# Kernel tuning notes

Hardware: AMD Instinct MI355X
Metric: run time of the kernel (lower is better)

Reference implementation:

```python
import jax, jax.numpy as jnp
import numpy as np

B, G, N = 32, 512, 512          # batch, group (POMO rollouts), problem size
EMB, H, DK = 128, 8, 16          # embedding_dim, head_num, qkv_dim (H*DK == EMB)
E, FH, K = 8, 512, 2             # num_experts, ff_hidden_dim, top-k
SQRT_EMB = 11.313708498984761    # sqrt(128), model_params['sqrt_embedding_dim']
CLIP = 10.0                      # logit_clipping


def setup_inputs() -> dict:
    key = jax.random.key(0)
    ks = jax.random.split(key, 22)
    s = 0.05
    d = {}
    d["pref"] = jax.random.uniform(ks[0], (2,), dtype=jnp.float32)
    d["graph"] = jax.random.normal(ks[1], (B, 1, EMB), dtype=jnp.float32)
    d["capacity"] = jax.random.uniform(ks[2], (B, G), dtype=jnp.float32)
    d["encoded_nodes"] = jax.random.normal(ks[3], (B, N, EMB), dtype=jnp.float32)
    d["ninf_mask"] = jnp.zeros((B, G, N), dtype=jnp.float32)
    # hyper-network MLP (note: original has NO activations between hyper_fc layers)
    d["fc1_w"] = jax.random.normal(ks[4], (256, 2)) * s
    d["fc1_b"] = jax.random.normal(ks[5], (256,)) * s
    d["fc2_w"] = jax.random.normal(ks[6], (256, 256)) * s
    d["fc2_b"] = jax.random.normal(ks[7], (256,)) * s
    d["fc3_w"] = jax.random.normal(ks[8], (8, 256)) * s
    d["fc3_b"] = jax.random.normal(ks[9], (8,)) * s
    # hyper heads producing the attention weight matrices (Linear(embd_dim=2, out), no bias)
    d["hWq"] = jax.random.normal(ks[10], ((1 + EMB) * H * DK, 2)) * 0.02
    d["hWk"] = jax.random.normal(ks[11], (EMB * H * DK, 2)) * 0.02
    d["hWv"] = jax.random.normal(ks[12], (EMB * H * DK, 2)) * 0.02
    d["hWc"] = jax.random.normal(ks[13], (EMB * H * DK, 2)) * 0.02
    # MoE combine layer: gating (token input + 8-dim pref embedding) and E expert MLPs
    d["gate_w"] = jax.random.normal(ks[14], (H * DK, E)) * s
    d["gate_pref_w"] = jax.random.normal(ks[15], (8, E)) * s
    d["e_w1"] = jax.random.normal(ks[16], (E, FH, H * DK)) * (1.0 / np.sqrt(H * DK))
    d["e_b1"] = jnp.zeros((E, FH), dtype=jnp.float32)
    d["e_w2"] = jax.random.normal(ks[17], (E, EMB, FH)) * (1.0 / np.sqrt(FH))
    d["e_b2"] = jnp.zeros((E, EMB), dtype=jnp.float32)
    d = {k2: v.astype(jnp.float32) for k2, v in d.items()}
    return d


def _heads(x):  # [B, n, H*DK] -> [B, H, n, DK]
    b, n, _ = x.shape
    return x.reshape(b, n, H, DK).transpose(0, 2, 1, 3)


def reference(pref, graph, capacity, encoded_nodes, ninf_mask,
              fc1_w, fc1_b, fc2_w, fc2_b, fc3_w, fc3_b,
              hWq, hWk, hWv, hWc,
              gate_w, gate_pref_w, e_w1, e_b1, e_w2, e_b2):
    # ---- assign(pref): hypernet generates attention weight matrices ----
    h = fc1_w @ pref + fc1_b
    h = fc2_w @ h + fc2_b
    mid = fc3_w @ h + fc3_b                      # [8] == mid_embd_pref
    Wq = (hWq @ mid[0:2]).reshape(H * DK, 1 + EMB)
    Wk = (hWk @ mid[2:4]).reshape(H * DK, EMB)
    Wv = (hWv @ mid[4:6]).reshape(H * DK, EMB)
    Wc = (hWc @ mid[6:8]).reshape(H * DK, EMB)
    # ---- set_kv ----
    k = _heads(encoded_nodes @ Wk.T)             # [B,H,N,DK]
    v = _heads(encoded_nodes @ Wv.T)
    # ---- forward ----
    inp = jnp.concatenate(
        [jnp.broadcast_to(graph, (B, G, EMB)), capacity[:, :, None]], axis=2)
    q = _heads(inp @ Wq.T)                       # [B,H,G,DK]
    score = jnp.einsum('bhgd,bhnd->bhgn', q, k) / jnp.sqrt(jnp.float32(DK))
    score = score + ninf_mask[:, None, :, :]
    attn = jax.nn.softmax(score, axis=3)
    out = jnp.einsum('bhgn,bhnd->bhgd', attn, v)
    out = out.transpose(0, 2, 1, 3).reshape(B, G, H * DK)   # [B,G,128]
    # ---- MoE combine (noisy top-k gating, deterministic at inference) ----
    logits = out @ gate_w + mid @ gate_pref_w    # [B,G,E]
    vals, idx = jax.lax.top_k(logits, K)
    gv = jax.nn.softmax(vals, axis=-1)           # softmax over selected k (T=1)
    gates = jnp.sum(jax.nn.one_hot(idx, E, dtype=out.dtype) * gv[..., None], axis=-2)
    hdn = jax.nn.relu(jnp.einsum('bgi,ehi->bgeh', out, e_w1) + e_b1)
    y = jnp.einsum('bgeh,eoh->bgeo', hdn, e_w2) + e_b2
    moe_out = jnp.einsum('bgeo,bge->bgo', y, gates)          # [B,G,EMB]
    # ---- combine + tanh-clipped masked softmax over nodes ----
    mh = moe_out @ Wc.T                           # [B,G,EMB]
    sc = jnp.einsum('bge,bne->bgn', mh, encoded_nodes) / SQRT_EMB
    probs = jax.nn.softmax(CLIP * jnp.tanh(sc) + ninf_mask, axis=2)
    return probs
```

## Files before the change

### kernel.cpp

```cpp
#include <hip/hip_runtime.h>


typedef __attribute__((ext_vector_type(8))) __bf16 bf16x8;
typedef __attribute__((ext_vector_type(4))) float f32x4;

static constexpr long OFF_MID   = 0;
static constexpr long OFF_PREFL = 8;
static constexpr long OFF_WL    = 16;
static constexpr long OFF_WKB   = 256;
static constexpr long OFF_WVB   = 8448;
static constexpr long OFF_WCB   = 16640;
static constexpr long OFF_QB    = 24832;
static constexpr long OFF_CNT   = 28928;
static constexpr long OFF_TOK   = 28936;
static constexpr long OFF_WGT   = 160008;
static constexpr long OFF_AO    = 291080;
static constexpr long OFF_MH    = 2388232;
static constexpr long OFF_ENCB  = 3436808;

__device__ __forceinline__ unsigned f2bf(float x) {
  union { float f; unsigned u; } v; v.f = x;
  return ((v.u + 0x7FFFu + ((v.u >> 16) & 1u)) >> 16) & 0xFFFFu;
}

__global__ __launch_bounds__(256)
void k_prep(const float* __restrict__ pref, const float* __restrict__ fc1w,
            const float* __restrict__ fc1b, const float* __restrict__ fc2w,
            const float* __restrict__ fc2b, const float* __restrict__ fc3w,
            const float* __restrict__ fc3b, const float* __restrict__ gpw,
            const float* __restrict__ graph,
            const float* __restrict__ hWq, const float* __restrict__ hWk,
            const float* __restrict__ hWv, const float* __restrict__ hWc,
            const float* __restrict__ ew1, const float* __restrict__ ew2,
            const float* __restrict__ enc,
            unsigned short* __restrict__ w1b, unsigned short* __restrict__ w2b,
            unsigned short* __restrict__ encb, float* __restrict__ ws) {
  const int bid = blockIdx.x;
  const int tid = threadIdx.x;
  if (bid < 3072) {
    const int i = bid*256 + tid;
    const float* src;
    unsigned short* dst;
    if (i < 131072)      { src = ew1 + (long)i*4;          dst = w1b + (long)i*4; }
    else if (i < 262144) { src = ew2 + (long)(i-131072)*4; dst = w2b + (long)(i-131072)*4; }
    else                 { src = enc + (long)(i-262144)*4; dst = encb + (long)(i-262144)*4; }
    const float4 v = *(const float4*)src;
    uint2 p;
    p.x = f2bf(v.x) | (f2bf(v.y) << 16);
    p.y = f2bf(v.z) | (f2bf(v.w) << 16);
    *(uint2*)dst = p;
    return;
  }
  __shared__ float h1[256];
  __shared__ float h2[256];
  __shared__ float mid[8];
  __shared__ float g[2][128];
  const float p0 = pref[0], p1 = pref[1];
  h1[tid] = fc1w[2*tid]*p0 + fc1w[2*tid+1]*p1 + fc1b[tid];
  __syncthreads();
  float s = 0.f;
  for (int j = 0; j < 256; ++j) s = fmaf(fc2w[tid*256+j], h1[j], s);
  h2[tid] = s + fc2b[tid];
  __syncthreads();
  if (tid < 8) {
    float s2 = 0.f;
    for (int j = 0; j < 256; ++j) s2 = fmaf(fc3w[tid*256+j], h2[j], s2);
    mid[tid] = s2 + fc3b[tid];
  }
  __syncthreads();
  if (bid < 3264) {
    const int i = (bid - 3072)*256 + tid;
    if (i < 16384) {
      ((unsigned short*)(ws + OFF_WKB))[i] =
          (unsigned short)f2bf(hWk[2*i]*mid[2] + hWk[2*i+1]*mid[3]);
    } else if (i < 32768) {
      const int j = i - 16384;
      ((unsigned short*)(ws + OFF_WVB))[j] =
          (unsigned short)f2bf(hWv[2*j]*mid[4] + hWv[2*j+1]*mid[5]);
    } else {
      const int j = i - 32768;
      ((unsigned short*)(ws + OFF_WCB))[j] =
          (unsigned short)f2bf(hWc[2*j]*mid[6] + hWc[2*j+1]*mid[7]);
    }
    return;
  }
  const int qb = bid - 3264;
  const int b0 = qb*2;
  {
    const int bb = tid >> 7, ii = tid & 127;
    g[bb][ii] = graph[(b0+bb)*128 + ii];
  }
  __syncthreads();
  const float m0 = mid[0], m1 = mid[1];
  {
    const int bb = tid >> 7, o = tid & 127;
    const float* hq = hWq + (long)o*129*2;
    float acc = 0.f;
    for (int i2 = 0; i2 < 128; ++i2) {
      const float w = hq[2*i2]*m0 + hq[2*i2+1]*m1;
      acc = fmaf(g[bb][i2], w, acc);
    }
    ws[OFF_QB + (b0+bb)*128 + o] = acc;
  }
  if (qb == 0) {
    if (tid < 8) {
      ws[OFF_MID + tid] = mid[tid];
      float s3 = 0.f;
      for (int i2 = 0; i2 < 8; ++i2) s3 = fmaf(mid[i2], gpw[i2*8 + tid], s3);
      ws[OFF_PREFL + tid] = s3;
      ((int*)(ws + OFF_CNT))[tid] = 0;
    }
    if (tid >= 16 && tid < 144) {
      const int o = tid - 16;
      ws[OFF_WL + o] = hWq[((long)o*129 + 128)*2]*m0 + hWq[((long)o*129 + 128)*2 + 1]*m1;
    }
  }
}

__device__ __forceinline__ bf16x8 ld_frag(const unsigned short* base, int row, int bytecol) {
  const int addr = row*256 + (bytecol ^ ((row & 7) << 4));
  return *(const bf16x8*)((const char*)base + addr);
}

__global__ __launch_bounds__(256)
void k_kv(const unsigned short* __restrict__ encb,
          const unsigned short* __restrict__ wkb,
          const unsigned short* __restrict__ wvb,
          unsigned short* __restrict__ Kb, unsigned short* __restrict__ Vb) {
  __shared__ unsigned short Ws[128*128];
  __shared__ unsigned short Xs[64*128];
  const int tid = threadIdx.x;
  const int nbase = blockIdx.x * 64;
  const unsigned short* Wb = blockIdx.y ? wvb : wkb;
  unsigned short* Cb = blockIdx.y ? Vb : Kb;
#pragma unroll
  for (int s = 0; s < 8; ++s) {
    const int id = tid + s*256;
    const int fr = id >> 4, c16 = id & 15;
    const uint4 v = *(const uint4*)(Wb + (long)fr*128 + c16*8);
    *(uint4*)((char*)Ws + fr*256 + ((c16*16) ^ ((fr & 7) << 4))) = v;
  }
#pragma unroll
  for (int s = 0; s < 4; ++s) {
    const int id = tid + s*256;
    const int r = id >> 4, c16 = id & 15;
    const uint4 v = *(const uint4*)(encb + (long)(nbase + r)*128 + c16*8);
    *(uint4*)((char*)Xs + r*256 + ((c16*16) ^ ((r & 7) << 4))) = v;
  }
  __syncthreads();
  const int w = tid >> 6, l = tid & 63, lq = l >> 4, lr = l & 15;
  f32x4 acc[2][4];
#pragma unroll
  for (int a = 0; a < 2; ++a)
#pragma unroll
    for (int m = 0; m < 4; ++m) acc[a][m] = (f32x4){0.f, 0.f, 0.f, 0.f};
#pragma unroll
  for (int ks = 0; ks < 4; ++ks) {
    const int bcol = ks*64 + lq*16;
    const bf16x8 a0 = ld_frag(Ws, (2*w  )*16 + lr, bcol);
    const bf16x8 a1 = ld_frag(Ws, (2*w+1)*16 + lr, bcol);
    const bf16x8 b0 = ld_frag(Xs, 0*16 + lr, bcol);
    const bf16x8 b1 = ld_frag(Xs, 1*16 + lr, bcol);
    const bf16x8 b2 = ld_frag(Xs, 2*16 + lr, bcol);
    const bf16x8 b3 = ld_frag(Xs, 3*16 + lr, bcol);
    acc[0][0] = __builtin_amdgcn_mfma_f32_16x16x32_bf16(a0, b0, acc[0][0], 0, 0, 0);
    acc[0][1] = __builtin_amdgcn_mfma_f32_16x16x32_bf16(a0, b1, acc[0][1], 0, 0, 0);
    acc[0][2] = __builtin_amdgcn_mfma_f32_16x16x32_bf16(a0, b2, acc[0][2], 0, 0, 0);
    acc[0][3] = __builtin_amdgcn_mfma_f32_16x16x32_bf16(a0, b3, acc[0][3], 0, 0, 0);
    acc[1][0] = __builtin_amdgcn_mfma_f32_16x16x32_bf16(a1, b0, acc[1][0], 0, 0, 0);
    acc[1][1] = __builtin_amdgcn_mfma_f32_16x16x32_bf16(a1, b1, acc[1][1], 0, 0, 0);
    acc[1][2] = __builtin_amdgcn_mfma_f32_16x16x32_bf16(a1, b2, acc[1][2], 0, 0, 0);
    acc[1][3] = __builtin_amdgcn_mfma_f32_16x16x32_bf16(a1, b3, acc[1][3], 0, 0, 0);
  }
#pragma unroll
  for (int obi = 0; obi < 2; ++obi) {
    const int o0 = (2*w + obi)*16 + lq*4;
#pragma unroll
    for (int mb = 0; mb < 4; ++mb) {
      const long n = nbase + mb*16 + lr;
      uint2 pp;
      pp.x = f2bf(acc[obi][mb][0]) | (f2bf(acc[obi][mb][1]) << 16);
      pp.y = f2bf(acc[obi][mb][2]) | (f2bf(acc[obi][mb][3]) << 16);
      *(uint2*)(Cb + n*128 + o0) = pp;
    }
  }
}

__global__ __launch_bounds__(256)
void k_mh(const float* __restrict__ Y0, const float* __restrict__ Y1,
          const unsigned short* __restrict__ wcb,
          unsigned short* __restrict__ mhb) {
  __shared__ unsigned short Ws[128*128];
  __shared__ unsigned short Xs[64*128];
  const int tid = threadIdx.x;
  const int nbase = blockIdx.x * 64;
#pragma unroll
  for (int s = 0; s < 8; ++s) {
    const int id = tid + s*256;
    const int fr = id >> 4, c16 = id & 15;
    const uint4 v = *(const uint4*)(wcb + (long)fr*128 + c16*8);
    *(uint4*)((char*)Ws + fr*256 + ((c16*16) ^ ((fr & 7) << 4))) = v;
  }
#pragma unroll
  for (int s = 0; s < 4; ++s) {
    const int id = tid + s*256;
    const int r = id >> 4, c16 = id & 15;
    const long base = (long)(nbase + r)*128 + c16*8;
    const float4 a0 = *(const float4*)(Y0 + base);
    const float4 a1 = *(const float4*)(Y0 + base + 4);
    const float4 b0 = *(const float4*)(Y1 + base);
    const float4 b1 = *(const float4*)(Y1 + base + 4);
    uint4 p;
    p.x = f2bf(a0.x + b0.x) | (f2bf(a0.y + b0.y) << 16);
    p.y = f2bf(a0.z + b0.z) | (f2bf(a0.w + b0.w) << 16);
    p.z = f2bf(a1.x + b1.x) | (f2bf(a1.y + b1.y) << 16);
    p.w = f2bf(a1.z + b1.z) | (f2bf(a1.w + b1.w) << 16);
    *(uint4*)((char*)Xs + r*256 + ((c16*16) ^ ((r & 7) << 4))) = p;
  }
  __syncthreads();
  const int w = tid >> 6, l = tid & 63, lq = l >> 4, lr = l & 15;
  f32x4 acc[2][4];
#pragma unroll
  for (int a = 0; a < 2; ++a)
#pragma unroll
    for (int m = 0; m < 4; ++m) acc[a][m] = (f32x4){0.f, 0.f, 0.f, 0.f};
#pragma unroll
  for (int ks = 0; ks < 4; ++ks) {
    const int bcol = ks*64 + lq*16;
    const bf16x8 a0 = ld_frag(Ws, (2*w  )*16 + lr, bcol);
    const bf16x8 a1 = ld_frag(Ws, (2*w+1)*16 + lr, bcol);
    const bf16x8 b0 = ld_frag(Xs, 0*16 + lr, bcol);
    const bf16x8 b1 = ld_frag(Xs, 1*16 + lr, bcol);
    const bf16x8 b2 = ld_frag(Xs, 2*16 + lr, bcol);
    const bf16x8 b3 = ld_frag(Xs, 3*16 + lr, bcol);
    acc[0][0] = __builtin_amdgcn_mfma_f32_16x16x32_bf16(a0, b0, acc[0][0], 0, 0, 0);
    acc[0][1] = __builtin_amdgcn_mfma_f32_16x16x32_bf16(a0, b1, acc[0][1], 0, 0, 0);
    acc[0][2] = __builtin_amdgcn_mfma_f32_16x16x32_bf16(a0, b2, acc[0][2], 0, 0, 0);
    acc[0][3] = __builtin_amdgcn_mfma_f32_16x16x32_bf16(a0, b3, acc[0][3], 0, 0, 0);
    acc[1][0] = __builtin_amdgcn_mfma_f32_16x16x32_bf16(a1, b0, acc[1][0], 0, 0, 0);
    acc[1][1] = __builtin_amdgcn_mfma_f32_16x16x32_bf16(a1, b1, acc[1][1], 0, 0, 0);
    acc[1][2] = __builtin_amdgcn_mfma_f32_16x16x32_bf16(a1, b2, acc[1][2], 0, 0, 0);
    acc[1][3] = __builtin_amdgcn_mfma_f32_16x16x32_bf16(a1, b3, acc[1][3], 0, 0, 0);
  }
#pragma unroll
  for (int obi = 0; obi < 2; ++obi) {
    const int o0 = (2*w + obi)*16 + lq*4;
#pragma unroll
    for (int mb = 0; mb < 4; ++mb) {
      const long n = nbase + mb*16 + lr;
      uint2 pp;
      pp.x = f2bf(acc[obi][mb][0]) | (f2bf(acc[obi][mb][1]) << 16);
      pp.y = f2bf(acc[obi][mb][2]) | (f2bf(acc[obi][mb][3]) << 16);
      *(uint2*)(mhb + n*128 + o0) = pp;
    }
  }
}

__global__ __launch_bounds__(512, 8)
void k_attn(const unsigned short* __restrict__ Kb,
            const unsigned short* __restrict__ Vb,
            const float* __restrict__ ws, const float* __restrict__ cap,
            const float* __restrict__ mask, float* __restrict__ AO) {
  const int bid = blockIdx.x;
  const int b = bid & 31, h = (bid >> 5) & 7, qh = bid >> 8;
  __shared__ unsigned short Kbf[512*16];
  __shared__ unsigned short Vt[16*512];
  __shared__ unsigned short Ps[8*16*32];
  const int tid = threadIdx.x;
#pragma unroll
  for (int it = 0; it < 2; ++it) {
    const int i = tid + it*512;
    const int n = i >> 1, hf = i & 1;
    const long src = (long)(b*512 + n)*128 + h*16 + hf*8;
    const uint4 kv = *(const uint4*)(Kb + src);
    *(uint4*)(Kbf + n*16 + hf*8) = kv;
    const uint4 vv = *(const uint4*)(Vb + src);
    const unsigned short* sp = (const unsigned short*)&vv;
#pragma unroll
    for (int j = 0; j < 8; ++j) {
      const int d = hf*8 + j;
      Vt[d*512 + (n ^ ((d & 7) << 3))] = sp[j];
    }
  }
  const int w = tid >> 6, l = tid & 63;
  const int lq = l >> 4, lr = l & 15;
  const int grow = qh*128 + w*16 + lr;
  bf16x8 qf;
  {
    union { uint4 u; bf16x8 v; } cv;
    cv.u = make_uint4(0u, 0u, 0u, 0u);
    if (lq < 2) {
      const float* qbp = ws + OFF_QB + b*128 + h*16 + lq*8;
      const float* wlp = ws + OFF_WL + h*16 + lq*8;
      const float cp = cap[b*512 + grow];
      float qv[8];
#pragma unroll
      for (int j = 0; j < 8; ++j) qv[j] = (qbp[j] + cp*wlp[j]) * 0.25f;
      cv.u.x = f2bf(qv[0]) | (f2bf(qv[1]) << 16);
      cv.u.y = f2bf(qv[2]) | (f2bf(qv[3]) << 16);
      cv.u.z = f2bf(qv[4]) | (f2bf(qv[5]) << 16);
      cv.u.w = f2bf(qv[6]) | (f2bf(qv[7]) << 16);
    }
    qf = cv.v;
  }
  unsigned short* Pw = Ps + w*16*32;
  const int psw = (lr & 3) << 3;
  __syncthreads();
  float m = -3.0e38f, lsum = 0.f;
  f32x4 oacc = {0.f, 0.f, 0.f, 0.f};
  const float* mrow = mask + ((long)(b*512 + grow))*512 + lq*4;
  for (int qc = 0; qc < 16; ++qc) {
    const int n0 = qc*32;
    f32x4 s[2];
#pragma unroll
    for (int nb = 0; nb < 2; ++nb) {
      bf16x8 kf;
      {
        union { uint4 u; bf16x8 v; } cv;
        cv.u = make_uint4(0u, 0u, 0u, 0u);
        if (lq < 2) cv.u = *(const uint4*)(Kbf + (n0 + nb*16 + lr)*16 + lq*8);
        kf = cv.v;
      }
      s[nb] = __builtin_amdgcn_mfma_f32_16x16x32_bf16(
          kf, qf, (f32x4){0.f, 0.f, 0.f, 0.f}, 0, 0, 0);
      const float4 mk = *(const float4*)(mrow + n0 + nb*16);
      s[nb][0] += mk.x; s[nb][1] += mk.y; s[nb][2] += mk.z; s[nb][3] += mk.w;
    }
    f32x4 mx;
    mx[0] = fmaxf(s[0][0], s[1][0]); mx[1] = fmaxf(s[0][1], s[1][1]);
    mx[2] = fmaxf(s[0][2], s[1][2]); mx[3] = fmaxf(s[0][3], s[1][3]);
    float cm = fmaxf(fmaxf(mx[0], mx[1]), fmaxf(mx[2], mx[3]));
    cm = fmaxf(cm, __shfl_xor(cm, 16));
    cm = fmaxf(cm, __shfl_xor(cm, 32));
    const float nm = fmaxf(m, cm);
    const float rs = __expf(m - nm);
    lsum *= rs;
    oacc[0] *= rs; oacc[1] *= rs; oacc[2] *= rs; oacc[3] *= rs;
    m = nm;
    float ls = 0.f;
#pragma unroll
    for (int nb = 0; nb < 2; ++nb) {
      const float e0 = __expf(s[nb][0] - m);
      const float e1 = __expf(s[nb][1] - m);
      const float e2 = __expf(s[nb][2] - m);
      const float e3 = __expf(s[nb][3] - m);
      ls += (e0 + e1) + (e2 + e3);
      uint2 pp;
      asm("v_cvt_pk_bf16_f32 %0, %1, %2" : "=v"(pp.x) : "v"(e0), "v"(e1));
      asm("v_cvt_pk_bf16_f32 %0, %1, %2" : "=v"(pp.y) : "v"(e2), "v"(e3));
      *(uint2*)(Pw + lr*32 + ((nb*16 + lq*4) ^ psw)) = pp;
    }
    lsum += ls;
    const bf16x8 va = *(const bf16x8*)(Vt + lr*512 + ((n0 + lq*8) ^ ((lr & 7) << 3)));
    const bf16x8 pb = *(const bf16x8*)(Pw + lr*32 + ((lq*8) ^ psw));
    oacc = __builtin_amdgcn_mfma_f32_16x16x32_bf16(va, pb, oacc, 0, 0, 0);
  }
  lsum += __shfl_xor(lsum, 16);
  lsum += __shfl_xor(lsum, 32);
  const float inv = 1.f / lsum;
  float4 o;
  o.x = oacc[0]*inv; o.y = oacc[1]*inv; o.z = oacc[2]*inv; o.w = oacc[3]*inv;
  *(float4*)(AO + (long)(b*512 + grow)*128 + h*16 + lq*4) = o;
}

__global__ __launch_bounds__(256)
void k_gate(const float* __restrict__ AO, const float* __restrict__ gw,
            float* __restrict__ ws) {
  const int tid = threadIdx.x;
  const int t = blockIdx.x*256 + tid;
  const float* x = AO + (long)t*128;
  float lg[8];
  {
    const float* pl = ws + OFF_PREFL;
#pragma unroll
    for (int e = 0; e < 8; ++e) lg[e] = pl[e];
  }
  for (int i = 0; i < 128; i += 4) {
    const float4 xv = *(const float4*)(x + i);
#pragma unroll
    for (int u = 0; u < 4; ++u) {
      const float xi = (&xv.x)[u];
      const float4 ga = *(const float4*)(gw + (i+u)*8);
      const float4 gb = *(const float4*)(gw + (i+u)*8 + 4);
      lg[0] = fmaf(xi, ga.x, lg[0]); lg[1] = fmaf(xi, ga.y, lg[1]);
      lg[2] = fmaf(xi, ga.z, lg[2]); lg[3] = fmaf(xi, ga.w, lg[3]);
      lg[4] = fmaf(xi, gb.x, lg[4]); lg[5] = fmaf(xi, gb.y, lg[5]);
      lg[6] = fmaf(xi, gb.z, lg[6]); lg[7] = fmaf(xi, gb.w, lg[7]);
    }
  }
  int i0 = 0; float v0 = lg[0];
#pragma unroll
  for (int e = 1; e < 8; ++e) if (lg[e] > v0) { v0 = lg[e]; i0 = e; }
  int i1 = -1; float v1 = -1e30f;
#pragma unroll
  for (int e = 0; e < 8; ++e) if (e != i0 && lg[e] > v1) { v1 = lg[e]; i1 = e; }
  const float e1 = __expf(v1 - v0);
  const float w0 = 1.f / (1.f + e1);
  const float w1 = 1.f - w0;
  __shared__ int bcnt[8];
  __shared__ int gbase[8];
  if (tid < 8) bcnt[tid] = 0;
  __syncthreads();
  const int p0 = atomicAdd(&bcnt[i0], 1);
  const int p1 = atomicAdd(&bcnt[i1], 1);
  __syncthreads();
  if (tid < 8) {
    int* cnt = (int*)(ws + OFF_CNT);
    gbase[tid] = (bcnt[tid] > 0) ? atomicAdd(&cnt[tid], bcnt[tid]) : 0;
  }
  __syncthreads();
  int* tokp = (int*)(ws + OFF_TOK);
  float* wgtp = ws + OFF_WGT;
  const int s0 = gbase[i0] + p0;
  tokp[i0*16384 + s0] = t;
  wgtp[i0*16384 + s0] = w0;
  const int s1 = gbase[i1] + p1;
  tokp[i1*16384 + s1] = t | (1 << 30);
  wgtp[i1*16384 + s1] = w1;
}

__global__ __launch_bounds__(256)
void k_moe(const float* __restrict__ AO,
           const unsigned short* __restrict__ w1b,
           const unsigned short* __restrict__ w2b,
           const float* __restrict__ eb1, const float* __restrict__ eb2,
           float* __restrict__ ws,
           float* __restrict__ Y0, float* __restrict__ Y1) {
  const int e = blockIdx.y;
  const int ce = ((const int*)(ws + OFF_CNT))[e];
  const int base = blockIdx.x * 64;
  if (base >= ce) return;
  const int nt = min(64, ce - base);

  __shared__ unsigned short Xs[64*128];
  __shared__ unsigned short Wts[128*128];
  __shared__ unsigned short Hs[64*128];
  __shared__ float seb1[512];
  __shared__ float seb2[128];
  __shared__ int   stok[64];
  __shared__ float swgt[64];

  const int tid = threadIdx.x;
  if (tid < 64) {
    if (tid < nt) {
      stok[tid] = ((const int*)(ws + OFF_TOK))[e*16384 + base + tid];
      swgt[tid] = (ws + OFF_WGT)[e*16384 + base + tid];
    } else { stok[tid] = -1; swgt[tid] = 0.f; }
  }
  for (int i = tid; i < 512; i += 256) seb1[i] = eb1[e*512 + i];
  if (tid < 128) seb2[tid] = eb2[e*128 + tid];
  __syncthreads();

#pragma unroll
  for (int r8 = 0; r8 < 8; ++r8) {
    const int id = tid + r8*256;
    const int r = id >> 5, c = id & 31;
    const int pk = stok[r];
    float4 xv = make_float4(0.f, 0.f, 0.f, 0.f);
    if (pk >= 0) xv = *(const float4*)(AO + (long)(pk & 0x3FFFFFFF)*128 + c*4);
    uint2 pkd;
    pkd.x = f2bf(xv.x) | (f2bf(xv.y) << 16);
    pkd.y = f2bf(xv.z) | (f2bf(xv.w) << 16);
    const int bc = (c*8) ^ ((r & 7) << 4);
    *(uint2*)((char*)Xs + r*256 + bc) = pkd;
  }

  const int w  = tid >> 6;
  const int l  = tid & 63;
  const int lq = l >> 4;
  const int lr = l & 15;

  f32x4 yacc[2][4];
#pragma unroll
  for (int a = 0; a < 2; ++a)
#pragma unroll
    for (int m = 0; m < 4; ++m) yacc[a][m] = (f32x4){0.f, 0.f, 0.f, 0.f};

  for (int fc = 0; fc < 4; ++fc) {
    __syncthreads();
    {
      const long wb = (long)(e*512 + fc*128) * 128;
#pragma unroll
      for (int s = 0; s < 8; ++s) {
        const int id = tid + s*256;
        const int fr = id >> 4, c16 = id & 15;
        const uint4 v = *(const uint4*)(w1b + wb + (long)fr*128 + c16*8);
        *(uint4*)((char*)Wts + fr*256 + ((c16*16) ^ ((fr & 7) << 4))) = v;
      }
    }
    __syncthreads();
    f32x4 hacc[2][4];
#pragma unroll
    for (int a = 0; a < 2; ++a)
#pragma unroll
      for (int m = 0; m < 4; ++m) hacc[a][m] = (f32x4){0.f, 0.f, 0.f, 0.f};
#pragma unroll
    for (int ks = 0; ks < 4; ++ks) {
      const int bcol = ks*64 + lq*16;
      const bf16x8 a0 = ld_frag(Wts, (2*w  )*16 + lr, bcol);
      const bf16x8 a1 = ld_frag(Wts, (2*w+1)*16 + lr, bcol);
      const bf16x8 b0 = ld_frag(Xs,  0*16 + lr, bcol);
      const bf16x8 b1 = ld_frag(Xs,  1*16 + lr, bcol);
      const bf16x8 b2 = ld_frag(Xs,  2*16 + lr, bcol);
      const bf16x8 b3 = ld_frag(Xs,  3*16 + lr, bcol);
      hacc[0][0] = __builtin_amdgcn_mfma_f32_16x16x32_bf16(a0, b0, hacc[0][0], 0, 0, 0);
      hacc[0][1] = __builtin_amdgcn_mfma_f32_16x16x32_bf16(a0, b1, hacc[0][1], 0, 0, 0);
      hacc[0][2] = __builtin_amdgcn_mfma_f32_16x16x32_bf16(a0, b2, hacc[0][2], 0, 0, 0);
      hacc[0][3] = __builtin_amdgcn_mfma_f32_16x16x32_bf16(a0, b3, hacc[0][3], 0, 0, 0);
      hacc[1][0] = __builtin_amdgcn_mfma_f32_16x16x32_bf16(a1, b0, hacc[1][0], 0, 0, 0);
      hacc[1][1] = __builtin_amdgcn_mfma_f32_16x16x32_bf16(a1, b1, hacc[1][1], 0, 0, 0);
      hacc[1][2] = __builtin_amdgcn_mfma_f32_16x16x32_bf16(a1, b2, hacc[1][2], 0, 0, 0);
      hacc[1][3] = __builtin_amdgcn_mfma_f32_16x16x32_bf16(a1, b3, hacc[1][3], 0, 0, 0);
    }
    __syncthreads();
#pragma unroll
    for (int fbi = 0; fbi < 2; ++fbi) {
      const int fb = (2*w + fbi)*16 + lq*4;
      const float4 bia = *(const float4*)&seb1[fc*128 + fb];
#pragma unroll
      for (int mb = 0; mb < 4; ++mb) {
        const int m = mb*16 + lr;
        const float h0 = fmaxf(hacc[fbi][mb][0] + bia.x, 0.f);
        const float h1 = fmaxf(hacc[fbi][mb][1] + bia.y, 0.f);
        const float h2 = fmaxf(hacc[fbi][mb][2] + bia.z, 0.f);
        const float h3 = fmaxf(hacc[fbi][mb][3] + bia.w, 0.f);
        uint2 p;
        p.x = f2bf(h0) | (f2bf(h1) << 16);
        p.y = f2bf(h2) | (f2bf(h3) << 16);
        const int bc = (fb*2) ^ ((m & 7) << 4);
        *(uint2*)((char*)Hs + m*256 + bc) = p;
      }
    }
    {
      const long wb = (long)(e*128) * 512 + fc*128;
#pragma unroll
      for (int s = 0; s < 8; ++s) {
        const int id = tid + s*256;
        const int orr = id >> 4, c16 = id & 15;
        const uint4 v = *(const uint4*)(w2b + wb + (long)orr*512 + c16*8);
        *(uint4*)((char*)Wts + orr*256 + ((c16*16) ^ ((orr & 7) << 4))) = v;
      }
    }
    __syncthreads();
#pragma unroll
    for (int ks = 0; ks < 4; ++ks) {
      const int bcol = ks*64 + lq*16;
      const bf16x8 a0 = ld_frag(Wts, (2*w  )*16 + lr, bcol);
      const bf16x8 a1 = ld_frag(Wts, (2*w+1)*16 + lr, bcol);
      const bf16x8 b0 = ld_frag(Hs,  0*16 + lr, bcol);
      const bf16x8 b1 = ld_frag(Hs,  1*16 + lr, bcol);
      const bf16x8 b2 = ld_frag(Hs,  2*16 + lr, bcol);
      const bf16x8 b3 = ld_frag(Hs,  3*16 + lr, bcol);
      yacc[0][0] = __builtin_amdgcn_mfma_f32_16x16x32_bf16(a0, b0, yacc[0][0], 0, 0, 0);
      yacc[0][1] = __builtin_amdgcn_mfma_f32_16x16x32_bf16(a0, b1, yacc[0][1], 0, 0, 0);
      yacc[0][2] = __builtin_amdgcn_mfma_f32_16x16x32_bf16(a0, b2, yacc[0][2], 0, 0, 0);
      yacc[0][3] = __builtin_amdgcn_mfma_f32_16x16x32_bf16(a0, b3, yacc[0][3], 0, 0, 0);
      yacc[1][0] = __builtin_amdgcn_mfma_f32_16x16x32_bf16(a1, b0, yacc[1][0], 0, 0, 0);
      yacc[1][1] = __builtin_amdgcn_mfma_f32_16x16x32_bf16(a1, b1, yacc[1][1], 0, 0, 0);
      yacc[1][2] = __builtin_amdgcn_mfma_f32_16x16x32_bf16(a1, b2, yacc[1][2], 0, 0, 0);
      yacc[1][3] = __builtin_amdgcn_mfma_f32_16x16x32_bf16(a1, b3, yacc[1][3], 0, 0, 0);
    }
  }
#pragma unroll
  for (int obi = 0; obi < 2; ++obi) {
    const int ob = (2*w + obi)*16 + lq*4;
    const float4 b2 = *(const float4*)&seb2[ob];
#pragma unroll
    for (int mb = 0; mb < 4; ++mb) {
      const int tl = mb*16 + lr;
      if (tl < nt) {
        const int pk = stok[tl];
        const int tk = pk & 0x3FFFFFFF;
        const float wgt = swgt[tl];
        float* Yp = ((pk >> 30) ? Y1 : Y0) + (long)tk*128 + ob;
        float4 o;
        o.x = (yacc[obi][mb][0] + b2.x) * wgt;
        o.y = (yacc[obi][mb][1] + b2.y) * wgt;
        o.z = (yacc[obi][mb][2] + b2.z) * wgt;
        o.w = (yacc[obi][mb][3] + b2.w) * wgt;
        *(float4*)Yp = o;
      }
    }
  }
}

__global__ __launch_bounds__(512)
void k_gemm2f(const unsigned short* __restrict__ mhb,
              const unsigned short* __restrict__ encb,
              const float* __restrict__ mask,
              float* __restrict__ out) {
  const int bid = blockIdx.x;
  const int b = bid & 31, rt = bid >> 5;
  __shared__ unsigned short Amh[64*128];
  __shared__ unsigned short Bch[512*32];
  __shared__ float red[64][9];
  const int tid = threadIdx.x;
  const int w = tid >> 6, l = tid & 63, lq = l >> 4, lr = l & 15;
  const long rowbase = (long)b*512 + rt*64;
#pragma unroll
  for (int s = 0; s < 2; ++s) {
    const int id = tid + s*512;
    const int r = id >> 4, c16 = id & 15;
    const uint4 v = *(const uint4*)(mhb + (rowbase + r)*128 + c16*8);
    *(uint4*)((char*)Amh + r*256 + ((c16*16) ^ ((r & 7) << 4))) = v;
  }
  f32x4 acc[4][4];
#pragma unroll
  for (int mi = 0; mi < 4; ++mi)
#pragma unroll
    for (int ni = 0; ni < 4; ++ni) acc[mi][ni] = (f32x4){0.f, 0.f, 0.f, 0.f};
  for (int kc = 0; kc < 4; ++kc) {
    __syncthreads();
#pragma unroll
    for (int s = 0; s < 4; ++s) {
      const int id = tid + s*512;
      const int n = id >> 2, sl = id & 3;
      const uint4 v = *(const uint4*)(encb + ((long)b*512 + n)*128 + kc*32 + sl*8);
      *(uint4*)((char*)Bch + n*64 + ((sl*16) ^ ((n & 3) << 4))) = v;
    }
    __syncthreads();
    bf16x8 af[4], bfr[4];
#pragma unroll
    for (int mi = 0; mi < 4; ++mi) {
      const int r = mi*16 + lr;
      af[mi] = *(const bf16x8*)((const char*)Amh + r*256 + ((kc*64 + lq*16) ^ ((r & 7) << 4)));
    }
#pragma unroll
    for (int ni = 0; ni < 4; ++ni) {
      const int n = w*64 + ni*16 + lr;
      bfr[ni] = *(const bf16x8*)((const char*)Bch + n*64 + ((lq*16) ^ ((n & 3) << 4)));
    }
#pragma unroll
    for (int mi = 0; mi < 4; ++mi)
#pragma unroll
      for (int ni = 0; ni < 4; ++ni)
        acc[mi][ni] = __builtin_amdgcn_mfma_f32_16x16x32_bf16(af[mi], bfr[ni], acc[mi][ni], 0, 0, 0);
  }
  const float ISC = 1.f/11.313708498984761f;
  float rsum[4][4];
#pragma unroll
  for (int mi = 0; mi < 4; ++mi)
#pragma unroll
    for (int j = 0; j < 4; ++j) rsum[mi][j] = 0.f;
#pragma unroll
  for (int mi = 0; mi < 4; ++mi) {
#pragma unroll
    for (int j = 0; j < 4; ++j) {
      const long row = rowbase + mi*16 + lq*4 + j;
      const float* mrow = mask + row*512 + w*64 + lr;
#pragma unroll
      for (int ni = 0; ni < 4; ++ni) {
        const float sc = acc[mi][ni][j] * ISC;
        const float li = 10.f*tanhf(sc) + mrow[ni*16];
        const float e = __expf(li - 10.f);
        acc[mi][ni][j] = e;
        rsum[mi][j] += e;
      }
    }
  }
#pragma unroll
  for (int mi = 0; mi < 4; ++mi)
#pragma unroll
    for (int j = 0; j < 4; ++j) {
#pragma unroll
      for (int o = 1; o < 16; o <<= 1) rsum[mi][j] += __shfl_xor(rsum[mi][j], o);
    }
  if (lr == 0) {
#pragma unroll
    for (int mi = 0; mi < 4; ++mi)
#pragma unroll
      for (int j = 0; j < 4; ++j) red[mi*16 + lq*4 + j][w] = rsum[mi][j];
  }
  __syncthreads();
  if (tid < 64) {
    float s = 0.f;
#pragma unroll
    for (int wv = 0; wv < 8; ++wv) s += red[tid][wv];
    red[tid][8] = 1.f / s;
  }
  __syncthreads();
#pragma unroll
  for (int mi = 0; mi < 4; ++mi) {
#pragma unroll
    for (int j = 0; j < 4; ++j) {
      const int rl = mi*16 + lq*4 + j;
      const float inv = red[rl][8];
      float* orow = out + (rowbase + rl)*512 + w*64 + lr;
#pragma unroll
      for (int ni = 0; ni < 4; ++ni) orow[ni*16] = acc[mi][ni][j] * inv;
    }
  }
}

extern "C" void kernel_launch(void* const* d_in, const int* in_sizes, int n_in,
                              void* d_out, int out_size, void* d_ws, size_t ws_size,
                              hipStream_t stream) {
  (void)in_sizes; (void)n_in; (void)out_size; (void)ws_size;
  const float* pref  = (const float*)d_in[0];
  const float* graph = (const float*)d_in[1];
  const float* cap   = (const float*)d_in[2];
  const float* enc   = (const float*)d_in[3];
  const float* mask  = (const float*)d_in[4];
  const float* fc1w  = (const float*)d_in[5];
  const float* fc1b  = (const float*)d_in[6];
  const float* fc2w  = (const float*)d_in[7];
  const float* fc2b  = (const float*)d_in[8];
  const float* fc3w  = (const float*)d_in[9];
  const float* fc3b  = (const float*)d_in[10];
  const float* hWq   = (const float*)d_in[11];
  const float* hWk   = (const float*)d_in[12];
  const float* hWv   = (const float*)d_in[13];
  const float* hWc   = (const float*)d_in[14];
  const float* gw    = (const float*)d_in[15];
  const float* gpw   = (const float*)d_in[16];
  const float* ew1   = (const float*)d_in[17];
  const float* eb1   = (const float*)d_in[18];
  const float* ew2   = (const float*)d_in[19];
  const float* eb2   = (const float*)d_in[20];
  float* ws  = (float*)d_ws;
  float* out = (float*)d_out;
  unsigned short* Kbuf = (unsigned short*)out;
  unsigned short* Vbuf = (unsigned short*)(out + 1048576);
  float* Y0 = out;
  float* Y1 = out + 2097152;
  unsigned short* ew1b = (unsigned short*)(out + 4194304);
  unsigned short* ew2b = (unsigned short*)(out + 4456448);
  unsigned short* mhb  = (unsigned short*)(ws + OFF_MH);
  unsigned short* encb = (unsigned short*)(ws + OFF_ENCB);
  unsigned short* wkb  = (unsigned short*)(ws + OFF_WKB);
  unsigned short* wvb  = (unsigned short*)(ws + OFF_WVB);
  unsigned short* wcb  = (unsigned short*)(ws + OFF_WCB);

  k_prep<<<3280, 256, 0, stream>>>(pref, fc1w, fc1b, fc2w, fc2b, fc3w, fc3b,
                                   gpw, graph, hWq, hWk, hWv, hWc,
                                   ew1, ew2, enc, ew1b, ew2b, encb, ws);
  k_kv<<<dim3(256, 2), 256, 0, stream>>>(encb, wkb, wvb, Kbuf, Vbuf);
  k_attn<<<1024, 512, 0, stream>>>(Kbuf, Vbuf, ws, cap, mask, ws + OFF_AO);
  k_gate<<<64, 256, 0, stream>>>(ws + OFF_AO, gw, ws);
  k_moe<<<dim3(256, 8), 256, 0, stream>>>(ws + OFF_AO, ew1b, ew2b, eb1, eb2, ws, Y0, Y1);
  k_mh<<<256, 256, 0, stream>>>(Y0, Y1, wcb, mhb);
  k_gemm2f<<<256, 512, 0, stream>>>(mhb, encb, mask, out);
}
```

Measured before the change: 127.7 us.

## Precompute per-row mask nonzero flags, skip mask loads in attention, pad LDS

Splits the prep kernel in two. The first kernel computes the hypernetwork MLP in one block, casts weights to bf16, and scans the ninf mask to record a per-row nonzero flag. The attention kernel reads these flags and skips its global mask loads for a wavefront whose rows are all zero. The K, V-transpose and P shared buffers switch from XOR swizzles to padded strides to avoid bank conflicts. This adds a full pass over the mask and an extra kernel launch, and it moves the hypernetwork work onto a single serial block ahead of the rest.

```diff
diff --git a/kernel.cpp b/kernel.cpp
--- a/kernel.cpp
+++ b/kernel.cpp
@@ -11,12 +11,13 @@
 static constexpr long OFF_WVB   = 8448;
 static constexpr long OFF_WCB   = 16640;
 static constexpr long OFF_QB    = 24832;
-static constexpr long OFF_CNT   = 28928;
-static constexpr long OFF_TOK   = 28936;
-static constexpr long OFF_WGT   = 160008;
-static constexpr long OFF_AO    = 291080;
-static constexpr long OFF_MH    = 2388232;
-static constexpr long OFF_ENCB  = 3436808;
+static constexpr long OFF_MFLAG = 28928;
+static constexpr long OFF_CNT   = 33024;
+static constexpr long OFF_TOK   = 33032;
+static constexpr long OFF_WGT   = 164104;
+static constexpr long OFF_AO    = 295176;
+static constexpr long OFF_MH    = 2392328;
+static constexpr long OFF_ENCB  = 3440904;
 
 __device__ __forceinline__ unsigned f2bf(float x) {
   union { float f; unsigned u; } v; v.f = x;
@@ -24,21 +25,50 @@
 }
 
 __global__ __launch_bounds__(256)
-void k_prep(const float* __restrict__ pref, const float* __restrict__ fc1w,
-            const float* __restrict__ fc1b, const float* __restrict__ fc2w,
-            const float* __restrict__ fc2b, const float* __restrict__ fc3w,
-            const float* __restrict__ fc3b, const float* __restrict__ gpw,
-            const float* __restrict__ graph,
-            const float* __restrict__ hWq, const float* __restrict__ hWk,
-            const float* __restrict__ hWv, const float* __restrict__ hWc,
-            const float* __restrict__ ew1, const float* __restrict__ ew2,
-            const float* __restrict__ enc,
-            unsigned short* __restrict__ w1b, unsigned short* __restrict__ w2b,
-            unsigned short* __restrict__ encb, float* __restrict__ ws) {
+void k_prep1(const float* __restrict__ pref, const float* __restrict__ fc1w,
+             const float* __restrict__ fc1b, const float* __restrict__ fc2w,
+             const float* __restrict__ fc2b, const float* __restrict__ fc3w,
+             const float* __restrict__ fc3b, const float* __restrict__ gpw,
+             const float* __restrict__ hWq, const float* __restrict__ mask,
+             const float* __restrict__ ew1, const float* __restrict__ ew2,
+             const float* __restrict__ enc,
+             unsigned short* __restrict__ w1b, unsigned short* __restrict__ w2b,
+             unsigned short* __restrict__ encb, float* __restrict__ ws) {
   const int bid = blockIdx.x;
   const int tid = threadIdx.x;
-  if (bid < 3072) {
-    const int i = bid*256 + tid;
+  if (bid == 0) {
+    __shared__ float h1[256];
+    __shared__ float h2[256];
+    __shared__ float mid[8];
+    const float p0 = pref[0], p1 = pref[1];
+    h1[tid] = fc1w[2*tid]*p0 + fc1w[2*tid+1]*p1 + fc1b[tid];
+    __syncthreads();
+    float s = 0.f;
+    for (int j = 0; j < 256; ++j) s = fmaf(fc2w[tid*256+j], h1[j], s);
+    h2[tid] = s + fc2b[tid];
+    __syncthreads();
+    if (tid < 8) {
+      float s2 = 0.f;
+      for (int j = 0; j < 256; ++j) s2 = fmaf(fc3w[tid*256+j], h2[j], s2);
+      mid[tid] = s2 + fc3b[tid];
+    }
+    __syncthreads();
+    if (tid < 8) {
+      ws[OFF_MID + tid] = mid[tid];
+      float s3 = 0.f;
+      for (int i = 0; i < 8; ++i) s3 = fmaf(mid[i], gpw[i*8 + tid], s3);
+      ws[OFF_PREFL + tid] = s3;
+      ((int*)(ws + OFF_CNT))[tid] = 0;
+    }
+    if (tid >= 16 && tid < 144) {
+      const int o = tid - 16;
+      ws[OFF_WL + o] = hWq[((long)o*129 + 128)*2]*mid[0]
+                     + hWq[((long)o*129 + 128)*2 + 1]*mid[1];
+    }
+    return;
+  }
+  if (bid <= 3072) {
+    const int i = (bid-1)*256 + tid;
     const float* src;
     unsigned short* dst;
     if (i < 131072)      { src = ew1 + (long)i*4;          dst = w1b + (long)i*4; }
@@ -51,25 +81,36 @@
     *(uint2*)dst = p;
     return;
   }
-  __shared__ float h1[256];
-  __shared__ float h2[256];
+  __shared__ int fl[8];
+  const int rowbase = (bid - 3073) * 8;
+  const int r = tid >> 5, seg = tid & 31;
+  if (tid < 8) fl[tid] = 0;
+  __syncthreads();
+  const float* mrow = mask + (long)(rowbase + r)*512 + seg*16;
+  int nz = 0;
+#pragma unroll
+  for (int c = 0; c < 4; ++c) {
+    const float4 v = *(const float4*)(mrow + c*4);
+    nz |= (v.x != 0.f) | (v.y != 0.f) | (v.z != 0.f) | (v.w != 0.f);
+  }
+  if (nz) atomicOr(&fl[r], 1);
+  __syncthreads();
+  if (tid < 8) ((char*)(ws + OFF_MFLAG))[rowbase + tid] = (char)fl[tid];
+}
+
+__global__ __launch_bounds__(256)
+void k_prep2(const float* __restrict__ graph,
+             const float* __restrict__ hWq, const float* __restrict__ hWk,
+             const float* __restrict__ hWv, const float* __restrict__ hWc,
+             float* __restrict__ ws) {
+  const int bid = blockIdx.x;
+  const int tid = threadIdx.x;
   __shared__ float mid[8];
   __shared__ float g[2][128];
-  const float p0 = pref[0], p1 = pref[1];
-  h1[tid] = fc1w[2*tid]*p0 + fc1w[2*tid+1]*p1 + fc1b[tid];
-  __syncthreads();
-  float s = 0.f;
-  for (int j = 0; j < 256; ++j) s = fmaf(fc2w[tid*256+j], h1[j], s);
-  h2[tid] = s + fc2b[tid];
-  __syncthreads();
-  if (tid < 8) {
-    float s2 = 0.f;
-    for (int j = 0; j < 256; ++j) s2 = fmaf(fc3w[tid*256+j], h2[j], s2);
-    mid[tid] = s2 + fc3b[tid];
-  }
-  __syncthreads();
-  if (bid < 3264) {
-    const int i = (bid - 3072)*256 + tid;
+  if (tid < 8) mid[tid] = ws[OFF_MID + tid];
+  __syncthreads();
+  if (bid < 192) {
+    const int i = bid*256 + tid;
     if (i < 16384) {
       ((unsigned short*)(ws + OFF_WKB))[i] =
           (unsigned short)f2bf(hWk[2*i]*mid[2] + hWk[2*i+1]*mid[3]);
@@ -84,7 +125,7 @@
     }
     return;
   }
-  const int qb = bid - 3264;
+  const int qb = bid - 192;
   const int b0 = qb*2;
   {
     const int bb = tid >> 7, ii = tid & 127;
@@ -92,29 +133,14 @@
   }
   __syncthreads();
   const float m0 = mid[0], m1 = mid[1];
-  {
-    const int bb = tid >> 7, o = tid & 127;
-    const float* hq = hWq + (long)o*129*2;
-    float acc = 0.f;
-    for (int i2 = 0; i2 < 128; ++i2) {
-      const float w = hq[2*i2]*m0 + hq[2*i2+1]*m1;
-      acc = fmaf(g[bb][i2], w, acc);
-    }
-    ws[OFF_QB + (b0+bb)*128 + o] = acc;
-  }
-  if (qb == 0) {
-    if (tid < 8) {
-      ws[OFF_MID + tid] = mid[tid];
-      float s3 = 0.f;
-      for (int i2 = 0; i2 < 8; ++i2) s3 = fmaf(mid[i2], gpw[i2*8 + tid], s3);
-      ws[OFF_PREFL + tid] = s3;
-      ((int*)(ws + OFF_CNT))[tid] = 0;
-    }
-    if (tid >= 16 && tid < 144) {
-      const int o = tid - 16;
-      ws[OFF_WL + o] = hWq[((long)o*129 + 128)*2]*m0 + hWq[((long)o*129 + 128)*2 + 1]*m1;
-    }
-  }
+  const int bb = tid >> 7, o = tid & 127;
+  const float* hq = hWq + (long)o*129*2;
+  float acc = 0.f;
+  for (int i2 = 0; i2 < 128; ++i2) {
+    const float w = hq[2*i2]*m0 + hq[2*i2+1]*m1;
+    acc = fmaf(g[bb][i2], w, acc);
+  }
+  ws[OFF_QB + (b0+bb)*128 + o] = acc;
 }
 
 __device__ __forceinline__ bf16x8 ld_frag(const unsigned short* base, int row, int bytecol) {
@@ -263,9 +289,9 @@
             const float* __restrict__ mask, float* __restrict__ AO) {
   const int bid = blockIdx.x;
   const int b = bid & 31, h = (bid >> 5) & 7, qh = bid >> 8;
-  __shared__ unsigned short Kbf[512*16];
-  __shared__ unsigned short Vt[16*512];
-  __shared__ unsigned short Ps[8*16*32];
+  __shared__ unsigned short Kbf[512*24];
+  __shared__ unsigned short Vt[16*536];
+  __shared__ unsigned short Ps[8*16*40];
   const int tid = threadIdx.x;
 #pragma unroll
   for (int it = 0; it < 2; ++it) {
@@ -273,14 +299,11 @@
     const int n = i >> 1, hf = i & 1;
     const long src = (long)(b*512 + n)*128 + h*16 + hf*8;
     const uint4 kv = *(const uint4*)(Kb + src);
-    *(uint4*)(Kbf + n*16 + hf*8) = kv;
+    *(uint4*)(Kbf + n*24 + hf*8) = kv;
     const uint4 vv = *(const uint4*)(Vb + src);
     const unsigned short* sp = (const unsigned short*)&vv;
 #pragma unroll
-    for (int j = 0; j < 8; ++j) {
-      const int d = hf*8 + j;
-      Vt[d*512 + (n ^ ((d & 7) << 3))] = sp[j];
-    }
+    for (int j = 0; j < 8; ++j) Vt[(hf*8 + j)*536 + n] = sp[j];
   }
   const int w = tid >> 6, l = tid & 63;
   const int lq = l >> 4, lr = l & 15;
@@ -303,7 +326,9 @@
     }
     qf = cv.v;
   }
-  unsigned short* Pw = Ps + w*16*32;
+  const int mf = ((const char*)(ws + OFF_MFLAG))[b*512 + grow];
+  const bool usemask = __any(mf != 0);
+  unsigned short* Pw = Ps + w*16*40;
   const int psw = (lr & 3) << 3;
   __syncthreads();
   float m = -3.0e38f, lsum = 0.f;
@@ -318,13 +343,15 @@
       {
         union { uint4 u; bf16x8 v; } cv;
         cv.u = make_uint4(0u, 0u, 0u, 0u);
-        if (lq < 2) cv.u = *(const uint4*)(Kbf + (n0 + nb*16 + lr)*16 + lq*8);
+        if (lq < 2) cv.u = *(const uint4*)(Kbf + (n0 + nb*16 + lr)*24 + lq*8);
         kf = cv.v;
       }
       s[nb] = __builtin_amdgcn_mfma_f32_16x16x32_bf16(
           kf, qf, (f32x4){0.f, 0.f, 0.f, 0.f}, 0, 0, 0);
-      const float4 mk = *(const float4*)(mrow + n0 + nb*16);
-      s[nb][0] += mk.x; s[nb][1] += mk.y; s[nb][2] += mk.z; s[nb][3] += mk.w;
+      if (usemask) {
+        const float4 mk = *(const float4*)(mrow + n0 + nb*16);
+        s[nb][0] += mk.x; s[nb][1] += mk.y; s[nb][2] += mk.z; s[nb][3] += mk.w;
+      }
     }
     f32x4 mx;
     mx[0] = fmaxf(s[0][0], s[1][0]); mx[1] = fmaxf(s[0][1], s[1][1]);
@@ -348,11 +375,11 @@
       uint2 pp;
       asm("v_cvt_pk_bf16_f32 %0, %1, %2" : "=v"(pp.x) : "v"(e0), "v"(e1));
       asm("v_cvt_pk_bf16_f32 %0, %1, %2" : "=v"(pp.y) : "v"(e2), "v"(e3));
-      *(uint2*)(Pw + lr*32 + ((nb*16 + lq*4) ^ psw)) = pp;
+      *(uint2*)(Pw + lr*40 + ((nb*16 + lq*4) ^ psw)) = pp;
     }
     lsum += ls;
-    const bf16x8 va = *(const bf16x8*)(Vt + lr*512 + ((n0 + lq*8) ^ ((lr & 7) << 3)));
-    const bf16x8 pb = *(const bf16x8*)(Pw + lr*32 + ((lq*8) ^ psw));
+    const bf16x8 va = *(const bf16x8*)(Vt + lr*536 + n0 + lq*8);
+    const bf16x8 pb = *(const bf16x8*)(Pw + lr*40 + (lq*8 ^ psw));
     oacc = __builtin_amdgcn_mfma_f32_16x16x32_bf16(va, pb, oacc, 0, 0, 0);
   }
   lsum += __shfl_xor(lsum, 16);
@@ -731,9 +758,10 @@
   unsigned short* wvb  = (unsigned short*)(ws + OFF_WVB);
   unsigned short* wcb  = (unsigned short*)(ws + OFF_WCB);
 
-  k_prep<<<3280, 256, 0, stream>>>(pref, fc1w, fc1b, fc2w, fc2b, fc3w, fc3b,
-                                   gpw, graph, hWq, hWk, hWv, hWc,
-                                   ew1, ew2, enc, ew1b, ew2b, encb, ws);
+  k_prep1<<<5121, 256, 0, stream>>>(pref, fc1w, fc1b, fc2w, fc2b, fc3w, fc3b,
+                                    gpw, hWq, mask, ew1, ew2, enc,
+                                    ew1b, ew2b, encb, ws);
+  k_prep2<<<208, 256, 0, stream>>>(graph, hWq, hWk, hWv, hWc, ws);
   k_kv<<<dim3(256, 2), 256, 0, stream>>>(encb, wkb, wvb, Kbuf, Vbuf);
   k_attn<<<1024, 512, 0, stream>>>(Kbuf, Vbuf, ws, cap, mask, ws + OFF_AO);
   k_gate<<<64, 256, 0, stream>>>(ws + OFF_AO, gw, ws);
```

After: 121.9 us. -4.5%, faster.
